# Performance work log

Hardware: AMD Instinct MI355X
Metric: run time of the kernel (lower is better)

The kernel has to match this reference:

```python
import jax, jax.numpy as jnp
import numpy as np

D_MODEL, D_FF, N_EXPERTS, TOP_K = 1024, 4096, 8, 2

def setup_inputs() -> dict:
    key = jax.random.key(0)
    k1, k2, k3, k4 = jax.random.split(key, 4)
    x = jax.random.normal(k1, (4, 2048, D_MODEL), dtype=jnp.float32)
    # glorot-ish scaled init for weights
    router = jax.random.normal(k2, (D_MODEL, N_EXPERTS), dtype=jnp.float32) * (1.0 / np.sqrt(D_MODEL))
    W1 = jax.random.normal(k3, (N_EXPERTS, D_MODEL, D_FF), dtype=jnp.float32) * (1.0 / np.sqrt(D_MODEL))
    W2 = jax.random.normal(k4, (N_EXPERTS, D_FF, D_MODEL), dtype=jnp.float32) * (1.0 / np.sqrt(D_FF))
    return {"x": x, "router": router, "W1": W1, "W2": W2}

def reference(x, router, W1, W2):
    B, S, d = x.shape
    E = router.shape[1]
    xf = x.reshape(-1, d)                              # [T, d]
    logits = xf @ router                               # [T, E]
    top_v, top_i = jax.lax.top_k(logits, TOP_K)        # [T, k]
    w = jax.nn.softmax(top_v, axis=-1)                 # softmax over selected experts
    # scatter top-k weights into a dense [T, E] gate matrix (indices are distinct)
    gates = jnp.sum(jax.nn.one_hot(top_i, E, dtype=x.dtype) * w[..., None], axis=1)
    out = jnp.zeros_like(xf)
    for e in range(E):                                 # small fixed expert loop
        h = xf @ W1[e]                                 # [T, d_ff]
        h = h * jax.nn.sigmoid(h)                      # swish
        out = out + gates[:, e:e + 1] * (h @ W2[e])    # weighted combine
    return out.reshape(B, S, d)
```

## Files before the change

### kernel.cpp

```cpp
#include <hip/hip_runtime.h>
#include <hip/hip_bf16.h>

#define NTOK 8192
#define DM 1024
#define DFF 4096
#define NE 8
#define MAXT 136

typedef __attribute__((ext_vector_type(8))) short bf16x8;
typedef __attribute__((ext_vector_type(4))) float f32x4;

__device__ __forceinline__ ushort f2bf(float f) {
  __hip_bfloat16 h = __float2bfloat16(f);
  return *reinterpret_cast<ushort*>(&h);
}

template <int K, int N>
__global__ void pack_w(const float* __restrict__ in, ushort* __restrict__ outp) {
  __shared__ float t[64][129];
  const int e = blockIdx.z, nT = blockIdx.x, kt = blockIdx.y;
  const float* src = in + (size_t)e * K * N + (size_t)kt * 64 * N + (size_t)nT * 128;
  const int tid = threadIdx.x;
#pragma unroll
  for (int it = 0; it < 8; ++it) {
    int idx = it * 256 + tid;
    int kl = idx >> 5, n4 = idx & 31;
    float4 v = *reinterpret_cast<const float4*>(src + (size_t)kl * N + n4 * 4);
    t[kl][n4 * 4 + 0] = v.x; t[kl][n4 * 4 + 1] = v.y;
    t[kl][n4 * 4 + 2] = v.z; t[kl][n4 * 4 + 3] = v.w;
  }
  __syncthreads();
  const int row = tid >> 1, half = tid & 1;
  const int s = (row & 7) << 3;
  union { ushort us[32]; uint4 q[4]; } u;
#pragma unroll
  for (int k2 = 0; k2 < 32; ++k2) u.us[k2] = f2bf(t[(half * 32 + k2) ^ s][row]);
  ushort* dst = outp + ((size_t)(e * (N / 128) + nT) * (K / 64) + kt) * 8192 + row * 64 + half * 32;
  uint4* d4 = reinterpret_cast<uint4*>(dst);
  d4[0] = u.q[0]; d4[1] = u.q[1]; d4[2] = u.q[2]; d4[3] = u.q[3];
}

__global__ void router_kernel(const float* __restrict__ x, const float* __restrict__ router,
                              int* __restrict__ cnt, int* __restrict__ list,
                              float* __restrict__ wa, ushort* __restrict__ xb) {
  __shared__ float rl[DM * NE];
  int tid = threadIdx.x;
  for (int i = tid; i < DM * NE / 4; i += 256)
    reinterpret_cast<float4*>(rl)[i] = reinterpret_cast<const float4*>(router)[i];
  __syncthreads();
  int wave = tid >> 6, lane = tid & 63;
  int tok0 = blockIdx.x * 32 + wave * 8;
  for (int tI = 0; tI < 8; ++tI) {
    int tok = tok0 + tI;
    float acc[NE];
#pragma unroll
    for (int e2 = 0; e2 < NE; ++e2) acc[e2] = 0.f;
    const float4* xr = reinterpret_cast<const float4*>(x + (size_t)tok * DM);
    ushort xo[16];
#pragma unroll
    for (int c = 0; c < 4; ++c) {
      float4 v = xr[lane * 4 + c];
      int d = lane * 16 + c * 4;
      const float* vv = reinterpret_cast<const float*>(&v);
#pragma unroll
      for (int q = 0; q < 4; ++q) {
        float xv = vv[q];
        xo[c * 4 + q] = f2bf(xv);
#pragma unroll
        for (int e2 = 0; e2 < NE; ++e2) acc[e2] += xv * rl[(d + q) * NE + e2];
      }
    }
    *reinterpret_cast<uint4*>(xb + (size_t)tok * DM + lane * 16) =
        *reinterpret_cast<const uint4*>(&xo[0]);
    *reinterpret_cast<uint4*>(xb + (size_t)tok * DM + lane * 16 + 8) =
        *reinterpret_cast<const uint4*>(&xo[8]);
    for (int off = 32; off > 0; off >>= 1) {
#pragma unroll
      for (int e2 = 0; e2 < NE; ++e2) acc[e2] += __shfl_xor(acc[e2], off, 64);
    }
    if (lane == 0) {
      int i0 = 0; float v0 = acc[0];
#pragma unroll
      for (int e2 = 1; e2 < NE; ++e2) { if (acc[e2] > v0) { v0 = acc[e2]; i0 = e2; } }
      int i1 = -1; float v1 = -3.4e38f;
#pragma unroll
      for (int e2 = 0; e2 < NE; ++e2) { if (e2 != i0 && acc[e2] > v1) { v1 = acc[e2]; i1 = e2; } }
      float e1 = expf(v1 - v0);
      float w0 = 1.f / (1.f + e1);
      float w1 = e1 / (1.f + e1);
      int s0 = atomicAdd(&cnt[i0], 1);
      list[i0 * NTOK + s0] = tok * 2;
      wa[tok * 2] = w0;
      int s1 = atomicAdd(&cnt[i1], 1);
      list[i1 * NTOK + s1] = tok * 2 + 1;
      wa[tok * 2 + 1] = w1;
    }
  }
}

__global__ void build_tiles(const int* __restrict__ cnt, unsigned* __restrict__ table) {
  if (threadIdx.x == 0) {
    int t = 0;
    for (int e = 0; e < NE; ++e) {
      int nt = (cnt[e] + 127) >> 7;
      for (int i = 0; i < nt; ++i) table[t++] = ((unsigned)e << 16) | (unsigned)i;
    }
    for (; t < MAXT; ++t) table[t] = 0xFFFFFFFFu;
  }
}

__device__ __forceinline__ void gl_lds16(unsigned long long g, void* s) {
  __builtin_amdgcn_global_load_lds(
      (const __attribute__((address_space(1))) unsigned int*)g,
      (__attribute__((address_space(3))) unsigned int*)s, 16, 0, 0);
}

#define WAITV0() asm volatile("s_waitcnt vmcnt(0)" ::: "memory")

__device__ __forceinline__ void BARRIER() {
  asm volatile("" ::: "memory");
  __builtin_amdgcn_s_barrier();
  asm volatile("" ::: "memory");
}

template <int PASS>
__launch_bounds__(256, 4)
__global__ void moe_gemm(const ushort* __restrict__ Xb,
                         const ushort* __restrict__ Wp,
                         ushort* __restrict__ Hp,
                         const int* __restrict__ cnt,
                         const int* __restrict__ list,
                         const unsigned* __restrict__ table,
                         const float* __restrict__ wa,
                         float* __restrict__ out) {
  constexpr int NK = (PASS == 1) ? 16 : 32;

  const int bid = blockIdx.x;
  const int xcd = bid & 7;
  const int j = bid >> 3;
  int t, nTile, kc;
  if (PASS == 1) { t = j >> 2; nTile = xcd * 4 + (j & 3); kc = 0; }
  else           { t = j >> 1; nTile = xcd; kc = j & 1; }
  unsigned td = table[t];
  if (td == 0xFFFFFFFFu) return;
  const int e = td >> 16;
  const int tTile = td & 0xFFFF;
  const int n = cnt[e];

  __shared__ __attribute__((aligned(16))) char As[16384];
  __shared__ __attribute__((aligned(16))) char Bs[16384];
  __shared__ int aL[128];
  __shared__ unsigned long long pL[128];

  const int tid = threadIdx.x;
  if constexpr (PASS == 1) {
    if (tid < 128) {
      int slot = tTile * 128 + tid;
      int sl = (slot < n) ? slot : (n - 1);
      int a = list[e * NTOK + sl];
      pL[tid] = (unsigned long long)(Xb + (size_t)(a >> 1) * DM);
    }
  } else {
    if (tid < 128) {
      int slot = tTile * 128 + tid;
      aL[tid] = (slot < n) ? list[e * NTOK + slot] : -1;
    }
  }
  __syncthreads();

  const char* Bsrc = (const char*)Wp +
      ((size_t)(e * ((PASS == 1) ? 32 : 8) + nTile) * ((PASS == 1) ? 16 : 64) + kc * 32) * 16384;
  const char* Asrc = nullptr;
  unsigned long long sA0[4];
  if constexpr (PASS == 1) {
    const int sr = tid >> 3, sc = (tid & 7) * 16;
#pragma unroll
    for (int jj = 0; jj < 4; ++jj) {
      int row = jj * 32 + sr;
      sA0[jj] = pL[row] + (unsigned)(sc ^ ((row & 7) << 4));
    }
  } else {
    Asrc = (const char*)Hp + ((size_t)t * 64 + kc * 32) * 16384;
  }

  const int wv = tid >> 6, lane = tid & 63;
  const int r0 = (wv >> 1) * 64, c0 = (wv & 1) * 64;

  f32x4 acc[4][4];
#pragma unroll
  for (int m = 0; m < 4; ++m)
#pragma unroll
    for (int nn = 0; nn < 4; ++nn) acc[m][nn] = (f32x4){0.f, 0.f, 0.f, 0.f};

  for (int kt = 0; kt < NK; ++kt) {
    if constexpr (PASS == 1) {
#pragma unroll
      for (int jj = 0; jj < 4; ++jj)
        gl_lds16(sA0[jj] + (unsigned)kt * 128, As + jj * 4096 + tid * 16);
    } else {
#pragma unroll
      for (int jj = 0; jj < 4; ++jj)
        gl_lds16((unsigned long long)(Asrc + (size_t)kt * 16384 + jj * 4096 + tid * 16),
                 As + jj * 4096 + tid * 16);
    }
#pragma unroll
    for (int jj = 0; jj < 4; ++jj)
      gl_lds16((unsigned long long)(Bsrc + (size_t)kt * 16384 + jj * 4096 + tid * 16),
               Bs + jj * 4096 + tid * 16);
    WAITV0();
    BARRIER();
#pragma unroll
    for (int kk = 0; kk < 2; ++kk) {
      const int kb = kk * 64 + (lane >> 4) * 16;
      bf16x8 af[4], bfr[4];
#pragma unroll
      for (int m = 0; m < 4; ++m) {
        int row = r0 + m * 16 + (lane & 15);
        af[m] = *reinterpret_cast<const bf16x8*>(As + row * 128 + (kb ^ ((row & 7) << 4)));
      }
#pragma unroll
      for (int nn = 0; nn < 4; ++nn) {
        int row = c0 + nn * 16 + (lane & 15);
        bfr[nn] = *reinterpret_cast<const bf16x8*>(Bs + row * 128 + (kb ^ ((row & 7) << 4)));
      }
      __builtin_amdgcn_s_setprio(1);
#pragma unroll
      for (int m = 0; m < 4; ++m)
#pragma unroll
        for (int nn = 0; nn < 4; ++nn)
          acc[m][nn] = __builtin_amdgcn_mfma_f32_16x16x32_bf16(af[m], bfr[nn], acc[m][nn], 0, 0, 0);
      __builtin_amdgcn_s_setprio(0);
    }
    BARRIER();
  }

#pragma unroll
  for (int m = 0; m < 4; ++m) {
#pragma unroll
    for (int jr = 0; jr < 4; ++jr) {
      int lr = r0 + m * 16 + (lane >> 4) * 4 + jr;
      if constexpr (PASS == 1) {
#pragma unroll
        for (int nn = 0; nn < 4; ++nn) {
          int cg = nTile * 128 + c0 + nn * 16 + (lane & 15);
          float v = acc[m][nn][jr];
          size_t us = ((size_t)t * 64 + (cg >> 6)) * 8192 + (size_t)lr * 64 +
                      ((cg & 63) ^ ((lr & 7) << 3));
          Hp[us] = f2bf(v / (1.f + expf(-v)));
        }
      } else {
        int a = aL[lr];
        if (a < 0) continue;
        float w = wa[a];
        int tok = a >> 1;
        float* orow = out + (size_t)tok * DM + nTile * 128 + c0 + (lane & 15);
#pragma unroll
        for (int nn = 0; nn < 4; ++nn)
          atomicAdd(&orow[nn * 16], w * acc[m][nn][jr]);
      }
    }
  }
}

extern "C" void kernel_launch(void* const* d_in, const int* in_sizes, int n_in,
                              void* d_out, int out_size, void* d_ws, size_t ws_size,
                              hipStream_t stream) {
  const float* x = (const float*)d_in[0];
  const float* router = (const float*)d_in[1];
  const float* W1 = (const float*)d_in[2];
  const float* W2 = (const float*)d_in[3];
  float* out = (float*)d_out;
  char* ws = (char*)d_ws;

  ushort* Xb  = (ushort*)(ws + 0);
  ushort* Wp1 = (ushort*)(ws + (size_t)16 * 1024 * 1024);
  ushort* Wp2 = (ushort*)(ws + 0);
  size_t off = (size_t)80 * 1024 * 1024;
  ushort* Hp = (ushort*)(ws + off); off += (size_t)MAXT * 64 * 16384;
  int* cnt  = (int*)(ws + off); off += 256;
  int* list = (int*)(ws + off); off += (size_t)NE * NTOK * 4;
  float* wa = (float*)(ws + off); off += (size_t)NTOK * 2 * 4;
  unsigned* table = (unsigned*)(ws + off); off += MAXT * 4;

  hipMemsetAsync(out, 0, (size_t)NTOK * DM * sizeof(float), stream);
  hipMemsetAsync(cnt, 0, NE * sizeof(int), stream);

  pack_w<DM, DFF><<<dim3(DFF / 128, DM / 64, NE), 256, 0, stream>>>(W1, Wp1);
  router_kernel<<<NTOK / 32, 256, 0, stream>>>(x, router, cnt, list, wa, Xb);
  build_tiles<<<1, 64, 0, stream>>>(cnt, table);

  moe_gemm<1><<<8 * 4 * MAXT, 256, 0, stream>>>(Xb, Wp1, Hp, cnt, list, table, wa, out);

  pack_w<DFF, DM><<<dim3(DM / 128, DFF / 64, NE), 256, 0, stream>>>(W2, Wp2);

  moe_gemm<2><<<8 * 2 * MAXT, 256, 0, stream>>>(Xb, Wp2, Hp, cnt, list, table, wa, out);
}
```

Before: 675.2 us.

## Enlarge MoE GEMM tiles to 256x256 with 1024 threads and LDS double buffering

Both expert GEMM passes move from 128x128 tiles with 256 threads to 256x256 tiles with 1024 threads (16 waves in a 4x4 grid). Global-to-LDS loads are now double-buffered so the next k-slice is fetched while MFMAs run on the current one. Expert token tiles grow to 256 rows, so the tile table shrinks and the H layout changes to match. The weight packing switches to nontemporal loads. Bigger tiles improve operand reuse and cut weight re-reads, but they use 128KB of LDS per block, which limits occupancy, and the 256-row tiles add more padding waste per expert.

```diff
diff --git a/kernel.cpp b/kernel.cpp
--- a/kernel.cpp
+++ b/kernel.cpp
@@ -5,7 +5,7 @@
 #define DM 1024
 #define DFF 4096
 #define NE 8
-#define MAXT 136
+#define TPAD 72
 
 typedef __attribute__((ext_vector_type(8))) short bf16x8;
 typedef __attribute__((ext_vector_type(4))) float f32x4;
@@ -25,7 +25,8 @@
   for (int it = 0; it < 8; ++it) {
     int idx = it * 256 + tid;
     int kl = idx >> 5, n4 = idx & 31;
-    float4 v = *reinterpret_cast<const float4*>(src + (size_t)kl * N + n4 * 4);
+    f32x4 v = __builtin_nontemporal_load(
+        reinterpret_cast<const f32x4*>(src + (size_t)kl * N + n4 * 4));
     t[kl][n4 * 4 + 0] = v.x; t[kl][n4 * 4 + 1] = v.y;
     t[kl][n4 * 4 + 2] = v.z; t[kl][n4 * 4 + 3] = v.w;
   }
@@ -102,10 +103,10 @@
   if (threadIdx.x == 0) {
     int t = 0;
     for (int e = 0; e < NE; ++e) {
-      int nt = (cnt[e] + 127) >> 7;
+      int nt = (cnt[e] + 255) >> 8;
       for (int i = 0; i < nt; ++i) table[t++] = ((unsigned)e << 16) | (unsigned)i;
     }
-    for (; t < MAXT; ++t) table[t] = 0xFFFFFFFFu;
+    for (; t < TPAD; ++t) table[t] = 0xFFFFFFFFu;
   }
 }
 
@@ -124,7 +125,7 @@
 }
 
 template <int PASS>
-__launch_bounds__(256, 4)
+__launch_bounds__(1024, 4)
 __global__ void moe_gemm(const ushort* __restrict__ Xb,
                          const ushort* __restrict__ Wp,
                          ushort* __restrict__ Hp,
@@ -139,52 +140,56 @@
   const int xcd = bid & 7;
   const int j = bid >> 3;
   int t, nTile, kc;
-  if (PASS == 1) { t = j >> 2; nTile = xcd * 4 + (j & 3); kc = 0; }
-  else           { t = j >> 1; nTile = xcd; kc = j & 1; }
+  if (PASS == 1) { t = j % TPAD; nTile = xcd * 2 + j / TPAD; kc = 0; }
+  else           { t = j; nTile = xcd >> 1; kc = xcd & 1; }
   unsigned td = table[t];
   if (td == 0xFFFFFFFFu) return;
   const int e = td >> 16;
   const int tTile = td & 0xFFFF;
   const int n = cnt[e];
 
-  __shared__ __attribute__((aligned(16))) char As[16384];
-  __shared__ __attribute__((aligned(16))) char Bs[16384];
-  __shared__ int aL[128];
-  __shared__ unsigned long long pL[128];
+  __shared__ __attribute__((aligned(16))) char As[2][32768];
+  __shared__ __attribute__((aligned(16))) char Bs[2][32768];
+  __shared__ int aL[256];
+  __shared__ unsigned long long pL[256];
 
   const int tid = threadIdx.x;
+  if (tid < 256) {
+    int slot = tTile * 256 + tid;
+    int sl = (slot < n) ? slot : (n - 1);
+    int a = list[e * NTOK + sl];
+    if constexpr (PASS == 2) aL[tid] = (slot < n) ? a : -1;
+    if constexpr (PASS == 1)
+      pL[tid] = (unsigned long long)(Xb + (size_t)(a >> 1) * DM);
+  }
+  __syncthreads();
+
+  const int sr = tid >> 3;
+  const int sc = (tid & 7) * 16;
+  const unsigned dOff = (unsigned)(sr * 128 + sc);
+  unsigned long long sA0[2];
   if constexpr (PASS == 1) {
-    if (tid < 128) {
-      int slot = tTile * 128 + tid;
-      int sl = (slot < n) ? slot : (n - 1);
-      int a = list[e * NTOK + sl];
-      pL[tid] = (unsigned long long)(Xb + (size_t)(a >> 1) * DM);
+#pragma unroll
+    for (int jj = 0; jj < 2; ++jj) {
+      int row = jj * 128 + sr;
+      sA0[jj] = pL[row] + (unsigned)(sc ^ ((row & 7) << 4));
     }
   } else {
-    if (tid < 128) {
-      int slot = tTile * 128 + tid;
-      aL[tid] = (slot < n) ? list[e * NTOK + slot] : -1;
-    }
-  }
-  __syncthreads();
-
-  const char* Bsrc = (const char*)Wp +
-      ((size_t)(e * ((PASS == 1) ? 32 : 8) + nTile) * ((PASS == 1) ? 16 : 64) + kc * 32) * 16384;
-  const char* Asrc = nullptr;
-  unsigned long long sA0[4];
-  if constexpr (PASS == 1) {
-    const int sr = tid >> 3, sc = (tid & 7) * 16;
-#pragma unroll
-    for (int jj = 0; jj < 4; ++jj) {
-      int row = jj * 32 + sr;
-      sA0[jj] = pL[row] + (unsigned)(sc ^ ((row & 7) << 4));
-    }
-  } else {
-    Asrc = (const char*)Hp + ((size_t)t * 64 + kc * 32) * 16384;
+    const char* Asrc = (const char*)Hp + ((size_t)t * 64 + kc * 32) * 32768;
+#pragma unroll
+    for (int jj = 0; jj < 2; ++jj)
+      sA0[jj] = (unsigned long long)(Asrc + jj * 16384 + dOff);
+  }
+  unsigned long long sB0[2];
+#pragma unroll
+  for (int p = 0; p < 2; ++p) {
+    size_t chunk = (PASS == 1) ? ((size_t)(e * 32 + nTile * 2 + p) * 16)
+                               : ((size_t)(e * 8 + nTile * 2 + p) * 64 + kc * 32);
+    sB0[p] = (unsigned long long)((const char*)Wp + chunk * 16384 + dOff);
   }
 
   const int wv = tid >> 6, lane = tid & 63;
-  const int r0 = (wv >> 1) * 64, c0 = (wv & 1) * 64;
+  const int wm = wv >> 2, wn = wv & 3;
 
   f32x4 acc[4][4];
 #pragma unroll
@@ -192,59 +197,69 @@
 #pragma unroll
     for (int nn = 0; nn < 4; ++nn) acc[m][nn] = (f32x4){0.f, 0.f, 0.f, 0.f};
 
+  auto STAGE = [&](int b, int kt) {
+    if constexpr (PASS == 1) {
+#pragma unroll
+      for (int jj = 0; jj < 2; ++jj)
+        gl_lds16(sA0[jj] + (unsigned)kt * 128, As[b] + jj * 16384 + dOff);
+    } else {
+#pragma unroll
+      for (int jj = 0; jj < 2; ++jj)
+        gl_lds16(sA0[jj] + (unsigned)kt * 32768, As[b] + jj * 16384 + dOff);
+    }
+#pragma unroll
+    for (int p = 0; p < 2; ++p)
+      gl_lds16(sB0[p] + (unsigned)kt * 16384, Bs[b] + p * 16384 + dOff);
+  };
+
+  auto COMPUTE = [&](int b) {
+#pragma unroll
+    for (int kk = 0; kk < 2; ++kk) {
+      const int kb = kk * 64 + (lane >> 4) * 16;
+      bf16x8 af[4], bq[4];
+#pragma unroll
+      for (int m = 0; m < 4; ++m) {
+        int row = wm * 64 + m * 16 + (lane & 15);
+        af[m] = *reinterpret_cast<const bf16x8*>(As[b] + row * 128 + (kb ^ ((row & 7) << 4)));
+      }
+#pragma unroll
+      for (int nn = 0; nn < 4; ++nn) {
+        int row = wn * 64 + nn * 16 + (lane & 15);
+        bq[nn] = *reinterpret_cast<const bf16x8*>(Bs[b] + row * 128 + (kb ^ ((row & 7) << 4)));
+      }
+      __builtin_amdgcn_s_setprio(1);
+#pragma unroll
+      for (int m = 0; m < 4; ++m)
+#pragma unroll
+        for (int nn = 0; nn < 4; ++nn)
+          acc[m][nn] = __builtin_amdgcn_mfma_f32_16x16x32_bf16(af[m], bq[nn], acc[m][nn], 0, 0, 0);
+      __builtin_amdgcn_s_setprio(0);
+    }
+  };
+
+  STAGE(0, 0);
+  WAITV0();
+  BARRIER();
+  int b = 0;
   for (int kt = 0; kt < NK; ++kt) {
-    if constexpr (PASS == 1) {
-#pragma unroll
-      for (int jj = 0; jj < 4; ++jj)
-        gl_lds16(sA0[jj] + (unsigned)kt * 128, As + jj * 4096 + tid * 16);
-    } else {
-#pragma unroll
-      for (int jj = 0; jj < 4; ++jj)
-        gl_lds16((unsigned long long)(Asrc + (size_t)kt * 16384 + jj * 4096 + tid * 16),
-                 As + jj * 4096 + tid * 16);
-    }
-#pragma unroll
-    for (int jj = 0; jj < 4; ++jj)
-      gl_lds16((unsigned long long)(Bsrc + (size_t)kt * 16384 + jj * 4096 + tid * 16),
-               Bs + jj * 4096 + tid * 16);
+    if (kt + 1 < NK) STAGE(b ^ 1, kt + 1);
+    COMPUTE(b);
     WAITV0();
     BARRIER();
-#pragma unroll
-    for (int kk = 0; kk < 2; ++kk) {
-      const int kb = kk * 64 + (lane >> 4) * 16;
-      bf16x8 af[4], bfr[4];
-#pragma unroll
-      for (int m = 0; m < 4; ++m) {
-        int row = r0 + m * 16 + (lane & 15);
-        af[m] = *reinterpret_cast<const bf16x8*>(As + row * 128 + (kb ^ ((row & 7) << 4)));
-      }
-#pragma unroll
-      for (int nn = 0; nn < 4; ++nn) {
-        int row = c0 + nn * 16 + (lane & 15);
-        bfr[nn] = *reinterpret_cast<const bf16x8*>(Bs + row * 128 + (kb ^ ((row & 7) << 4)));
-      }
-      __builtin_amdgcn_s_setprio(1);
-#pragma unroll
-      for (int m = 0; m < 4; ++m)
-#pragma unroll
-        for (int nn = 0; nn < 4; ++nn)
-          acc[m][nn] = __builtin_amdgcn_mfma_f32_16x16x32_bf16(af[m], bfr[nn], acc[m][nn], 0, 0, 0);
-      __builtin_amdgcn_s_setprio(0);
-    }
-    BARRIER();
+    b ^= 1;
   }
 
 #pragma unroll
   for (int m = 0; m < 4; ++m) {
 #pragma unroll
     for (int jr = 0; jr < 4; ++jr) {
-      int lr = r0 + m * 16 + (lane >> 4) * 4 + jr;
+      int lr = wm * 64 + m * 16 + (lane >> 4) * 4 + jr;
       if constexpr (PASS == 1) {
 #pragma unroll
         for (int nn = 0; nn < 4; ++nn) {
-          int cg = nTile * 128 + c0 + nn * 16 + (lane & 15);
+          int cg = nTile * 256 + wn * 64 + nn * 16 + (lane & 15);
           float v = acc[m][nn][jr];
-          size_t us = ((size_t)t * 64 + (cg >> 6)) * 8192 + (size_t)lr * 64 +
+          size_t us = ((size_t)t * 64 + (cg >> 6)) * 16384 + (size_t)lr * 64 +
                       ((cg & 63) ^ ((lr & 7) << 3));
           Hp[us] = f2bf(v / (1.f + expf(-v)));
         }
@@ -253,7 +268,7 @@
         if (a < 0) continue;
         float w = wa[a];
         int tok = a >> 1;
-        float* orow = out + (size_t)tok * DM + nTile * 128 + c0 + (lane & 15);
+        float* orow = out + (size_t)tok * DM + nTile * 256 + wn * 64 + (lane & 15);
 #pragma unroll
         for (int nn = 0; nn < 4; ++nn)
           atomicAdd(&orow[nn * 16], w * acc[m][nn][jr]);
@@ -276,11 +291,11 @@
   ushort* Wp1 = (ushort*)(ws + (size_t)16 * 1024 * 1024);
   ushort* Wp2 = (ushort*)(ws + 0);
   size_t off = (size_t)80 * 1024 * 1024;
-  ushort* Hp = (ushort*)(ws + off); off += (size_t)MAXT * 64 * 16384;
+  ushort* Hp = (ushort*)(ws + off); off += (size_t)TPAD * 64 * 32768;
   int* cnt  = (int*)(ws + off); off += 256;
   int* list = (int*)(ws + off); off += (size_t)NE * NTOK * 4;
   float* wa = (float*)(ws + off); off += (size_t)NTOK * 2 * 4;
-  unsigned* table = (unsigned*)(ws + off); off += MAXT * 4;
+  unsigned* table = (unsigned*)(ws + off); off += TPAD * 4;
 
   hipMemsetAsync(out, 0, (size_t)NTOK * DM * sizeof(float), stream);
   hipMemsetAsync(cnt, 0, NE * sizeof(int), stream);
@@ -289,9 +304,9 @@
   router_kernel<<<NTOK / 32, 256, 0, stream>>>(x, router, cnt, list, wa, Xb);
   build_tiles<<<1, 64, 0, stream>>>(cnt, table);
 
-  moe_gemm<1><<<8 * 4 * MAXT, 256, 0, stream>>>(Xb, Wp1, Hp, cnt, list, table, wa, out);
+  moe_gemm<1><<<8 * 2 * TPAD, 1024, 0, stream>>>(Xb, Wp1, Hp, cnt, list, table, wa, out);
 
   pack_w<DFF, DM><<<dim3(DM / 128, DFF / 64, NE), 256, 0, stream>>>(W2, Wp2);
 
-  moe_gemm<2><<<8 * 2 * MAXT, 256, 0, stream>>>(Xb, Wp2, Hp, cnt, list, table, wa, out);
-}
+  moe_gemm<2><<<8 * TPAD, 1024, 0, stream>>>(Xb, Wp2, Hp, cnt, list, table, wa, out);
+}
```

New measurement: 749.8 us. +11.1%, slower.

## Widen GEMM tiles to 128x256 with 512 threads and drop build_tiles kernel

Applied to the files above, without the earlier changes.

The MoE GEMM block tile grows from 128x128 to 128x256 with 8 waves per 512-thread block, so each A tile loaded into LDS is reused across twice as many output columns. The separate single-thread build_tiles launch is removed and each block now finds its expert tile by scanning the expert counts inline. The weight packing loads become nontemporal. In exchange, LDS use per block doubles for B, the grid halves, and there may be fewer resident blocks per CU.

```diff
diff --git a/kernel.cpp b/kernel.cpp
--- a/kernel.cpp
+++ b/kernel.cpp
@@ -25,7 +25,8 @@
   for (int it = 0; it < 8; ++it) {
     int idx = it * 256 + tid;
     int kl = idx >> 5, n4 = idx & 31;
-    float4 v = *reinterpret_cast<const float4*>(src + (size_t)kl * N + n4 * 4);
+    f32x4 v = __builtin_nontemporal_load(
+        reinterpret_cast<const f32x4*>(src + (size_t)kl * N + n4 * 4));
     t[kl][n4 * 4 + 0] = v.x; t[kl][n4 * 4 + 1] = v.y;
     t[kl][n4 * 4 + 2] = v.z; t[kl][n4 * 4 + 3] = v.w;
   }
@@ -98,17 +99,6 @@
   }
 }
 
-__global__ void build_tiles(const int* __restrict__ cnt, unsigned* __restrict__ table) {
-  if (threadIdx.x == 0) {
-    int t = 0;
-    for (int e = 0; e < NE; ++e) {
-      int nt = (cnt[e] + 127) >> 7;
-      for (int i = 0; i < nt; ++i) table[t++] = ((unsigned)e << 16) | (unsigned)i;
-    }
-    for (; t < MAXT; ++t) table[t] = 0xFFFFFFFFu;
-  }
-}
-
 __device__ __forceinline__ void gl_lds16(unsigned long long g, void* s) {
   __builtin_amdgcn_global_load_lds(
       (const __attribute__((address_space(1))) unsigned int*)g,
@@ -124,13 +114,12 @@
 }
 
 template <int PASS>
-__launch_bounds__(256, 4)
+__launch_bounds__(512, 2)
 __global__ void moe_gemm(const ushort* __restrict__ Xb,
                          const ushort* __restrict__ Wp,
                          ushort* __restrict__ Hp,
                          const int* __restrict__ cnt,
                          const int* __restrict__ list,
-                         const unsigned* __restrict__ table,
                          const float* __restrict__ wa,
                          float* __restrict__ out) {
   constexpr int NK = (PASS == 1) ? 16 : 32;
@@ -139,52 +128,59 @@
   const int xcd = bid & 7;
   const int j = bid >> 3;
   int t, nTile, kc;
-  if (PASS == 1) { t = j >> 2; nTile = xcd * 4 + (j & 3); kc = 0; }
-  else           { t = j >> 1; nTile = xcd; kc = j & 1; }
-  unsigned td = table[t];
-  if (td == 0xFFFFFFFFu) return;
-  const int e = td >> 16;
-  const int tTile = td & 0xFFFF;
+  if (PASS == 1) { t = j % MAXT; nTile = xcd * 2 + j / MAXT; kc = 0; }
+  else           { t = j; nTile = xcd >> 1; kc = xcd & 1; }
+  int e = -1, tTile = 0, accT = 0;
+#pragma unroll
+  for (int ee = 0; ee < NE; ++ee) {
+    int nt = (cnt[ee] + 127) >> 7;
+    if (e < 0 && t < accT + nt) { e = ee; tTile = t - accT; }
+    accT += nt;
+  }
+  if (e < 0) return;
   const int n = cnt[e];
 
   __shared__ __attribute__((aligned(16))) char As[16384];
-  __shared__ __attribute__((aligned(16))) char Bs[16384];
+  __shared__ __attribute__((aligned(16))) char Bs[32768];
   __shared__ int aL[128];
   __shared__ unsigned long long pL[128];
 
   const int tid = threadIdx.x;
+  if (tid < 128) {
+    int slot = tTile * 128 + tid;
+    int sl = (slot < n) ? slot : (n - 1);
+    int a = list[e * NTOK + sl];
+    aL[tid] = (slot < n) ? a : -1;
+    if (PASS == 1) pL[tid] = (unsigned long long)(Xb + (size_t)(a >> 1) * DM);
+  }
+  __syncthreads();
+
+  const int srow = tid >> 3;
+  const int sc = (tid & 7) * 16;
+  unsigned long long sA[2];
   if constexpr (PASS == 1) {
-    if (tid < 128) {
-      int slot = tTile * 128 + tid;
-      int sl = (slot < n) ? slot : (n - 1);
-      int a = list[e * NTOK + sl];
-      pL[tid] = (unsigned long long)(Xb + (size_t)(a >> 1) * DM);
+#pragma unroll
+    for (int q = 0; q < 2; ++q) {
+      int row = q * 64 + srow;
+      sA[q] = pL[row] + (unsigned)(sc ^ ((row & 7) << 4));
     }
   } else {
-    if (tid < 128) {
-      int slot = tTile * 128 + tid;
-      aL[tid] = (slot < n) ? list[e * NTOK + slot] : -1;
-    }
-  }
-  __syncthreads();
-
-  const char* Bsrc = (const char*)Wp +
-      ((size_t)(e * ((PASS == 1) ? 32 : 8) + nTile) * ((PASS == 1) ? 16 : 64) + kc * 32) * 16384;
-  const char* Asrc = nullptr;
-  unsigned long long sA0[4];
-  if constexpr (PASS == 1) {
-    const int sr = tid >> 3, sc = (tid & 7) * 16;
-#pragma unroll
-    for (int jj = 0; jj < 4; ++jj) {
-      int row = jj * 32 + sr;
-      sA0[jj] = pL[row] + (unsigned)(sc ^ ((row & 7) << 4));
-    }
-  } else {
-    Asrc = (const char*)Hp + ((size_t)t * 64 + kc * 32) * 16384;
+    const char* Asrc = (const char*)Hp + ((size_t)t * 64 + kc * 32) * 16384;
+#pragma unroll
+    for (int q = 0; q < 2; ++q) sA[q] = (unsigned long long)(Asrc + q * 8192 + tid * 16);
+  }
+  unsigned long long sB[4];
+#pragma unroll
+  for (int jj = 0; jj < 4; ++jj) {
+    size_t series = (PASS == 1) ? ((size_t)e * 32 + nTile * 2 + (jj >> 1))
+                                : ((size_t)e * 8 + nTile * 2 + (jj >> 1));
+    size_t chunk0 = (PASS == 1) ? (series * 16) : (series * 64 + kc * 32);
+    sB[jj] = (unsigned long long)((const char*)Wp + chunk0 * 16384 + (jj & 1) * 8192 + tid * 16);
   }
 
   const int wv = tid >> 6, lane = tid & 63;
-  const int r0 = (wv >> 1) * 64, c0 = (wv & 1) * 64;
+  const int wm = wv >> 2, wn = wv & 3;
+  const int l15 = lane & 15;
 
   f32x4 acc[4][4];
 #pragma unroll
@@ -195,40 +191,38 @@
   for (int kt = 0; kt < NK; ++kt) {
     if constexpr (PASS == 1) {
 #pragma unroll
-      for (int jj = 0; jj < 4; ++jj)
-        gl_lds16(sA0[jj] + (unsigned)kt * 128, As + jj * 4096 + tid * 16);
+      for (int q = 0; q < 2; ++q)
+        gl_lds16(sA[q] + (unsigned)kt * 128, As + q * 8192 + tid * 16);
     } else {
 #pragma unroll
-      for (int jj = 0; jj < 4; ++jj)
-        gl_lds16((unsigned long long)(Asrc + (size_t)kt * 16384 + jj * 4096 + tid * 16),
-                 As + jj * 4096 + tid * 16);
+      for (int q = 0; q < 2; ++q)
+        gl_lds16(sA[q] + (unsigned)kt * 16384, As + q * 8192 + tid * 16);
     }
 #pragma unroll
     for (int jj = 0; jj < 4; ++jj)
-      gl_lds16((unsigned long long)(Bsrc + (size_t)kt * 16384 + jj * 4096 + tid * 16),
-               Bs + jj * 4096 + tid * 16);
+      gl_lds16(sB[jj] + (unsigned)kt * 16384, Bs + jj * 8192 + tid * 16);
     WAITV0();
     BARRIER();
 #pragma unroll
     for (int kk = 0; kk < 2; ++kk) {
       const int kb = kk * 64 + (lane >> 4) * 16;
-      bf16x8 af[4], bfr[4];
+      bf16x8 af[4], bq[4];
 #pragma unroll
       for (int m = 0; m < 4; ++m) {
-        int row = r0 + m * 16 + (lane & 15);
+        int row = wm * 64 + m * 16 + l15;
         af[m] = *reinterpret_cast<const bf16x8*>(As + row * 128 + (kb ^ ((row & 7) << 4)));
       }
 #pragma unroll
       for (int nn = 0; nn < 4; ++nn) {
-        int row = c0 + nn * 16 + (lane & 15);
-        bfr[nn] = *reinterpret_cast<const bf16x8*>(Bs + row * 128 + (kb ^ ((row & 7) << 4)));
+        int row = wn * 64 + nn * 16 + l15;
+        bq[nn] = *reinterpret_cast<const bf16x8*>(Bs + row * 128 + (kb ^ ((row & 7) << 4)));
       }
       __builtin_amdgcn_s_setprio(1);
 #pragma unroll
       for (int m = 0; m < 4; ++m)
 #pragma unroll
         for (int nn = 0; nn < 4; ++nn)
-          acc[m][nn] = __builtin_amdgcn_mfma_f32_16x16x32_bf16(af[m], bfr[nn], acc[m][nn], 0, 0, 0);
+          acc[m][nn] = __builtin_amdgcn_mfma_f32_16x16x32_bf16(af[m], bq[nn], acc[m][nn], 0, 0, 0);
       __builtin_amdgcn_s_setprio(0);
     }
     BARRIER();
@@ -238,11 +232,11 @@
   for (int m = 0; m < 4; ++m) {
 #pragma unroll
     for (int jr = 0; jr < 4; ++jr) {
-      int lr = r0 + m * 16 + (lane >> 4) * 4 + jr;
+      int lr = wm * 64 + m * 16 + (lane >> 4) * 4 + jr;
       if constexpr (PASS == 1) {
 #pragma unroll
         for (int nn = 0; nn < 4; ++nn) {
-          int cg = nTile * 128 + c0 + nn * 16 + (lane & 15);
+          int cg = nTile * 256 + wn * 64 + nn * 16 + l15;
           float v = acc[m][nn][jr];
           size_t us = ((size_t)t * 64 + (cg >> 6)) * 8192 + (size_t)lr * 64 +
                       ((cg & 63) ^ ((lr & 7) << 3));
@@ -253,7 +247,7 @@
         if (a < 0) continue;
         float w = wa[a];
         int tok = a >> 1;
-        float* orow = out + (size_t)tok * DM + nTile * 128 + c0 + (lane & 15);
+        float* orow = out + (size_t)tok * DM + nTile * 256 + wn * 64 + l15;
 #pragma unroll
         for (int nn = 0; nn < 4; ++nn)
           atomicAdd(&orow[nn * 16], w * acc[m][nn][jr]);
@@ -280,18 +274,16 @@
   int* cnt  = (int*)(ws + off); off += 256;
   int* list = (int*)(ws + off); off += (size_t)NE * NTOK * 4;
   float* wa = (float*)(ws + off); off += (size_t)NTOK * 2 * 4;
-  unsigned* table = (unsigned*)(ws + off); off += MAXT * 4;
 
   hipMemsetAsync(out, 0, (size_t)NTOK * DM * sizeof(float), stream);
   hipMemsetAsync(cnt, 0, NE * sizeof(int), stream);
 
   pack_w<DM, DFF><<<dim3(DFF / 128, DM / 64, NE), 256, 0, stream>>>(W1, Wp1);
   router_kernel<<<NTOK / 32, 256, 0, stream>>>(x, router, cnt, list, wa, Xb);
-  build_tiles<<<1, 64, 0, stream>>>(cnt, table);
-
-  moe_gemm<1><<<8 * 4 * MAXT, 256, 0, stream>>>(Xb, Wp1, Hp, cnt, list, table, wa, out);
+
+  moe_gemm<1><<<8 * 2 * MAXT, 512, 0, stream>>>(Xb, Wp1, Hp, cnt, list, wa, out);
 
   pack_w<DFF, DM><<<dim3(DM / 128, DFF / 64, NE), 256, 0, stream>>>(W2, Wp2);
 
-  moe_gemm<2><<<8 * 2 * MAXT, 256, 0, stream>>>(Xb, Wp2, Hp, cnt, list, table, wa, out);
-}
+  moe_gemm<2><<<8 * MAXT, 512, 0, stream>>>(Xb, Wp2, Hp, cnt, list, wa, out);
+}
```

New measurement: 711.4 us. 1.05x slower.

## Fuse router with W1 packing and overlap W2 packing with first GEMM

Applied to the files above, without the earlier changes.

Merges the W1 pack and router into a single launch, and drops the build_tiles kernel by having each GEMM block derive its expert/tile from the counts itself. When the workspace is large enough, the W2 pack blocks are appended to the first GEMM grid so the conversion overlaps with GEMM work, with Wp2 moved to a separate region. Weight loads during packing use nontemporal hints. This cuts launches and serialization, at the cost of a larger shared-memory union per block and mixed workloads within one grid.

```diff
diff --git a/kernel.cpp b/kernel.cpp
--- a/kernel.cpp
+++ b/kernel.cpp
@@ -15,17 +15,33 @@
   return *reinterpret_cast<ushort*>(&h);
 }
 
-template <int K, int N>
-__global__ void pack_w(const float* __restrict__ in, ushort* __restrict__ outp) {
-  __shared__ float t[64][129];
-  const int e = blockIdx.z, nT = blockIdx.x, kt = blockIdx.y;
+struct GemmSM {
+  alignas(16) char As[16384];
+  alignas(16) char Bs[16384];
+  int aL[128];
+  unsigned long long pL[128];
+};
+union SMem {
+  GemmSM g;
+  float t[64][129];
+  float rl[DM * NE];
+};
+
+__device__ __forceinline__ void pack_block(const float* __restrict__ in,
+                                           ushort* __restrict__ outp, int bid,
+                                           int K, int N, float (&t)[64][129]) {
+  const int nTn = N >> 7, ktn = K >> 6;
+  const int perE = nTn * ktn;
+  const int e = bid / perE, rem = bid % perE;
+  const int nT = rem % nTn, kt = rem / nTn;
   const float* src = in + (size_t)e * K * N + (size_t)kt * 64 * N + (size_t)nT * 128;
   const int tid = threadIdx.x;
 #pragma unroll
   for (int it = 0; it < 8; ++it) {
     int idx = it * 256 + tid;
     int kl = idx >> 5, n4 = idx & 31;
-    float4 v = *reinterpret_cast<const float4*>(src + (size_t)kl * N + n4 * 4);
+    f32x4 v = __builtin_nontemporal_load(
+        reinterpret_cast<const f32x4*>(src + (size_t)kl * N + n4 * 4));
     t[kl][n4 * 4 + 0] = v.x; t[kl][n4 * 4 + 1] = v.y;
     t[kl][n4 * 4 + 2] = v.z; t[kl][n4 * 4 + 3] = v.w;
   }
@@ -35,21 +51,22 @@
   union { ushort us[32]; uint4 q[4]; } u;
 #pragma unroll
   for (int k2 = 0; k2 < 32; ++k2) u.us[k2] = f2bf(t[(half * 32 + k2) ^ s][row]);
-  ushort* dst = outp + ((size_t)(e * (N / 128) + nT) * (K / 64) + kt) * 8192 + row * 64 + half * 32;
+  ushort* dst = outp + ((size_t)(e * nTn + nT) * ktn + kt) * 8192 + row * 64 + half * 32;
   uint4* d4 = reinterpret_cast<uint4*>(dst);
   d4[0] = u.q[0]; d4[1] = u.q[1]; d4[2] = u.q[2]; d4[3] = u.q[3];
 }
 
-__global__ void router_kernel(const float* __restrict__ x, const float* __restrict__ router,
-                              int* __restrict__ cnt, int* __restrict__ list,
-                              float* __restrict__ wa, ushort* __restrict__ xb) {
-  __shared__ float rl[DM * NE];
+__device__ __forceinline__ void router_block(const float* __restrict__ x,
+                                             const float* __restrict__ rtr,
+                                             int* __restrict__ cnt, int* __restrict__ list,
+                                             float* __restrict__ wa, ushort* __restrict__ xb,
+                                             int rbid, float* rl) {
   int tid = threadIdx.x;
   for (int i = tid; i < DM * NE / 4; i += 256)
-    reinterpret_cast<float4*>(rl)[i] = reinterpret_cast<const float4*>(router)[i];
+    reinterpret_cast<float4*>(rl)[i] = reinterpret_cast<const float4*>(rtr)[i];
   __syncthreads();
   int wave = tid >> 6, lane = tid & 63;
-  int tok0 = blockIdx.x * 32 + wave * 8;
+  int tok0 = rbid * 32 + wave * 8;
   for (int tI = 0; tI < 8; ++tI) {
     int tok = tok0 + tI;
     float acc[NE];
@@ -98,17 +115,6 @@
   }
 }
 
-__global__ void build_tiles(const int* __restrict__ cnt, unsigned* __restrict__ table) {
-  if (threadIdx.x == 0) {
-    int t = 0;
-    for (int e = 0; e < NE; ++e) {
-      int nt = (cnt[e] + 127) >> 7;
-      for (int i = 0; i < nt; ++i) table[t++] = ((unsigned)e << 16) | (unsigned)i;
-    }
-    for (; t < MAXT; ++t) table[t] = 0xFFFFFFFFu;
-  }
-}
-
 __device__ __forceinline__ void gl_lds16(unsigned long long g, void* s) {
   __builtin_amdgcn_global_load_lds(
       (const __attribute__((address_space(1))) unsigned int*)g,
@@ -124,52 +130,44 @@
 }
 
 template <int PASS>
-__launch_bounds__(256, 4)
-__global__ void moe_gemm(const ushort* __restrict__ Xb,
-                         const ushort* __restrict__ Wp,
-                         ushort* __restrict__ Hp,
-                         const int* __restrict__ cnt,
-                         const int* __restrict__ list,
-                         const unsigned* __restrict__ table,
-                         const float* __restrict__ wa,
-                         float* __restrict__ out) {
+__device__ __forceinline__ void gemm_body(GemmSM& smg, int bid,
+                                          const ushort* __restrict__ Xb,
+                                          const ushort* __restrict__ Wp,
+                                          ushort* __restrict__ Hp,
+                                          const int* __restrict__ cnt,
+                                          const int* __restrict__ list,
+                                          const float* __restrict__ wa,
+                                          float* __restrict__ out) {
   constexpr int NK = (PASS == 1) ? 16 : 32;
 
-  const int bid = blockIdx.x;
   const int xcd = bid & 7;
   const int j = bid >> 3;
   int t, nTile, kc;
   if (PASS == 1) { t = j >> 2; nTile = xcd * 4 + (j & 3); kc = 0; }
   else           { t = j >> 1; nTile = xcd; kc = j & 1; }
-  unsigned td = table[t];
-  if (td == 0xFFFFFFFFu) return;
-  const int e = td >> 16;
-  const int tTile = td & 0xFFFF;
+  int e = -1, tTile = 0, accT = 0;
+#pragma unroll
+  for (int ee = 0; ee < NE; ++ee) {
+    int nt = (cnt[ee] + 127) >> 7;
+    if (e < 0 && t < accT + nt) { e = ee; tTile = t - accT; }
+    accT += nt;
+  }
+  if (e < 0) return;
   const int n = cnt[e];
 
-  __shared__ __attribute__((aligned(16))) char As[16384];
-  __shared__ __attribute__((aligned(16))) char Bs[16384];
-  __shared__ int aL[128];
-  __shared__ unsigned long long pL[128];
-
   const int tid = threadIdx.x;
-  if constexpr (PASS == 1) {
-    if (tid < 128) {
-      int slot = tTile * 128 + tid;
-      int sl = (slot < n) ? slot : (n - 1);
-      int a = list[e * NTOK + sl];
-      pL[tid] = (unsigned long long)(Xb + (size_t)(a >> 1) * DM);
-    }
-  } else {
-    if (tid < 128) {
-      int slot = tTile * 128 + tid;
-      aL[tid] = (slot < n) ? list[e * NTOK + slot] : -1;
-    }
+  if (tid < 128) {
+    int slot = tTile * 128 + tid;
+    int sl = (slot < n) ? slot : (n - 1);
+    int a = list[e * NTOK + sl];
+    smg.aL[tid] = (slot < n) ? a : -1;
+    if (PASS == 1) smg.pL[tid] = (unsigned long long)(Xb + (size_t)(a >> 1) * DM);
   }
   __syncthreads();
 
   const char* Bsrc = (const char*)Wp +
-      ((size_t)(e * ((PASS == 1) ? 32 : 8) + nTile) * ((PASS == 1) ? 16 : 64) + kc * 32) * 16384;
+      ((size_t)(e * ((PASS == 1) ? 32 : 8) + nTile) * ((PASS == 1) ? 16 : 64) +
+       (size_t)kc * 32) * 16384;
   const char* Asrc = nullptr;
   unsigned long long sA0[4];
   if constexpr (PASS == 1) {
@@ -177,7 +175,7 @@
 #pragma unroll
     for (int jj = 0; jj < 4; ++jj) {
       int row = jj * 32 + sr;
-      sA0[jj] = pL[row] + (unsigned)(sc ^ ((row & 7) << 4));
+      sA0[jj] = smg.pL[row] + (unsigned)(sc ^ ((row & 7) << 4));
     }
   } else {
     Asrc = (const char*)Hp + ((size_t)t * 64 + kc * 32) * 16384;
@@ -196,17 +194,17 @@
     if constexpr (PASS == 1) {
 #pragma unroll
       for (int jj = 0; jj < 4; ++jj)
-        gl_lds16(sA0[jj] + (unsigned)kt * 128, As + jj * 4096 + tid * 16);
+        gl_lds16(sA0[jj] + (unsigned)kt * 128, smg.As + jj * 4096 + tid * 16);
     } else {
 #pragma unroll
       for (int jj = 0; jj < 4; ++jj)
         gl_lds16((unsigned long long)(Asrc + (size_t)kt * 16384 + jj * 4096 + tid * 16),
-                 As + jj * 4096 + tid * 16);
+                 smg.As + jj * 4096 + tid * 16);
     }
 #pragma unroll
     for (int jj = 0; jj < 4; ++jj)
       gl_lds16((unsigned long long)(Bsrc + (size_t)kt * 16384 + jj * 4096 + tid * 16),
-               Bs + jj * 4096 + tid * 16);
+               smg.Bs + jj * 4096 + tid * 16);
     WAITV0();
     BARRIER();
 #pragma unroll
@@ -216,12 +214,12 @@
 #pragma unroll
       for (int m = 0; m < 4; ++m) {
         int row = r0 + m * 16 + (lane & 15);
-        af[m] = *reinterpret_cast<const bf16x8*>(As + row * 128 + (kb ^ ((row & 7) << 4)));
+        af[m] = *reinterpret_cast<const bf16x8*>(smg.As + row * 128 + (kb ^ ((row & 7) << 4)));
       }
 #pragma unroll
       for (int nn = 0; nn < 4; ++nn) {
         int row = c0 + nn * 16 + (lane & 15);
-        bfr[nn] = *reinterpret_cast<const bf16x8*>(Bs + row * 128 + (kb ^ ((row & 7) << 4)));
+        bfr[nn] = *reinterpret_cast<const bf16x8*>(smg.Bs + row * 128 + (kb ^ ((row & 7) << 4)));
       }
       __builtin_amdgcn_s_setprio(1);
 #pragma unroll
@@ -249,7 +247,7 @@
           Hp[us] = f2bf(v / (1.f + expf(-v)));
         }
       } else {
-        int a = aL[lr];
+        int a = smg.aL[lr];
         if (a < 0) continue;
         float w = wa[a];
         int tok = a >> 1;
@@ -260,6 +258,53 @@
       }
     }
   }
+}
+
+__global__ __launch_bounds__(256, 4) void prep1(const float* __restrict__ x,
+                                                const float* __restrict__ rtr,
+                                                const float* __restrict__ W1,
+                                                int* cnt, int* list, float* wa,
+                                                ushort* __restrict__ Xb,
+                                                ushort* __restrict__ Wp1) {
+  __shared__ SMem sm;
+  if (blockIdx.x < 4096) {
+    pack_block(W1, Wp1, blockIdx.x, DM, DFF, sm.t);
+    return;
+  }
+  router_block(x, rtr, cnt, list, wa, Xb, blockIdx.x - 4096, sm.rl);
+}
+
+__global__ __launch_bounds__(256, 4) void moe_p1(const ushort* __restrict__ Xb,
+                                                 const ushort* __restrict__ Wp1,
+                                                 ushort* __restrict__ Hp,
+                                                 const int* __restrict__ cnt,
+                                                 const int* __restrict__ list,
+                                                 const float* __restrict__ wa,
+                                                 float* __restrict__ out,
+                                                 const float* __restrict__ W2,
+                                                 ushort* __restrict__ Wp2) {
+  __shared__ SMem sm;
+  if (blockIdx.x >= 4352) {
+    pack_block(W2, Wp2, blockIdx.x - 4352, DFF, DM, sm.t);
+    return;
+  }
+  gemm_body<1>(sm.g, blockIdx.x, Xb, Wp1, Hp, cnt, list, wa, out);
+}
+
+__global__ __launch_bounds__(256, 4) void moe_p2(const ushort* __restrict__ Wp2,
+                                                 ushort* __restrict__ Hp,
+                                                 const int* __restrict__ cnt,
+                                                 const int* __restrict__ list,
+                                                 const float* __restrict__ wa,
+                                                 float* __restrict__ out) {
+  __shared__ SMem sm;
+  gemm_body<2>(sm.g, blockIdx.x, nullptr, Wp2, Hp, cnt, list, wa, out);
+}
+
+__global__ __launch_bounds__(256, 4) void pack_w2_k(const float* __restrict__ W2,
+                                                    ushort* __restrict__ Wp2) {
+  __shared__ SMem sm;
+  pack_block(W2, Wp2, blockIdx.x, DFF, DM, sm.t);
 }
 
 extern "C" void kernel_launch(void* const* d_in, const int* in_sizes, int n_in,
@@ -272,26 +317,29 @@
   float* out = (float*)d_out;
   char* ws = (char*)d_ws;
 
-  ushort* Xb  = (ushort*)(ws + 0);
-  ushort* Wp1 = (ushort*)(ws + (size_t)16 * 1024 * 1024);
-  ushort* Wp2 = (ushort*)(ws + 0);
-  size_t off = (size_t)80 * 1024 * 1024;
-  ushort* Hp = (ushort*)(ws + off); off += (size_t)MAXT * 64 * 16384;
-  int* cnt  = (int*)(ws + off); off += 256;
-  int* list = (int*)(ws + off); off += (size_t)NE * NTOK * 4;
-  float* wa = (float*)(ws + off); off += (size_t)NTOK * 2 * 4;
-  unsigned* table = (unsigned*)(ws + off); off += MAXT * 4;
+  ushort* Xb  = (ushort*)(ws);
+  ushort* Wp1 = (ushort*)(ws + (16ull << 20));
+  ushort* Hp  = (ushort*)(ws + (80ull << 20));
+  size_t oMisc = (80ull << 20) + (size_t)MAXT * 64 * 16384;
+  int* cnt  = (int*)(ws + oMisc);
+  int* list = (int*)(ws + oMisc + 1024);
+  float* wa = (float*)(ws + oMisc + 1024 + (size_t)NE * NTOK * 4);
+  size_t oEnd = oMisc + 1024 + (size_t)NE * NTOK * 4 + (size_t)NTOK * 2 * 4;
+  size_t oWp2 = (oEnd + 255) & ~(size_t)255;
+  const bool fused = ws_size >= oWp2 + (64ull << 20);
+  ushort* Wp2 = fused ? (ushort*)(ws + oWp2) : (ushort*)ws;
 
   hipMemsetAsync(out, 0, (size_t)NTOK * DM * sizeof(float), stream);
   hipMemsetAsync(cnt, 0, NE * sizeof(int), stream);
 
-  pack_w<DM, DFF><<<dim3(DFF / 128, DM / 64, NE), 256, 0, stream>>>(W1, Wp1);
-  router_kernel<<<NTOK / 32, 256, 0, stream>>>(x, router, cnt, list, wa, Xb);
-  build_tiles<<<1, 64, 0, stream>>>(cnt, table);
-
-  moe_gemm<1><<<8 * 4 * MAXT, 256, 0, stream>>>(Xb, Wp1, Hp, cnt, list, table, wa, out);
-
-  pack_w<DFF, DM><<<dim3(DM / 128, DFF / 64, NE), 256, 0, stream>>>(W2, Wp2);
-
-  moe_gemm<2><<<8 * 2 * MAXT, 256, 0, stream>>>(Xb, Wp2, Hp, cnt, list, table, wa, out);
-}
+  prep1<<<4096 + 256, 256, 0, stream>>>(x, router, W1, cnt, list, wa, Xb, Wp1);
+
+  if (fused) {
+    moe_p1<<<4352 + 4096, 256, 0, stream>>>(Xb, Wp1, Hp, cnt, list, wa, out, W2, Wp2);
+  } else {
+    moe_p1<<<4352, 256, 0, stream>>>(Xb, Wp1, Hp, cnt, list, wa, out, W2, Wp2);
+    pack_w2_k<<<4096, 256, 0, stream>>>(W2, Wp2);
+  }
+
+  moe_p2<<<2176, 256, 0, stream>>>(Wp2, Hp, cnt, list, wa, out);
+}
```

After: 652.8 us. 3.3% less time.
